# Performance work log

Hardware: AMD Instinct MI355X
Metric: run time of the kernel (lower is better)

Reference implementation:

```python
import jax, jax.numpy as jnp
import numpy as np

D_MODEL = 1024
NUM_HEADS = 16
DEPTH = D_MODEL // NUM_HEADS
LN_EPS = 1e-5


def setup_inputs() -> dict:
    key = jax.random.key(0)
    ks = jax.random.split(key, 12)
    B, S, D = 4, 2048, D_MODEL
    s = 1.0 / np.sqrt(D)
    inp = {
        "Q": jax.random.normal(ks[0], (B, S, D), jnp.float32),
        "K": jax.random.normal(ks[1], (B, S, D), jnp.float32),
        "V": jax.random.normal(ks[2], (B, S, D), jnp.float32),
        "mask": jnp.ones((B, 1, 1, S), jnp.int32),
        "Wq": jax.random.normal(ks[3], (D, D), jnp.float32) * s,
        "bq": jnp.zeros((D,), jnp.float32),
        "Wk": jax.random.normal(ks[4], (D, D), jnp.float32) * s,
        "bk": jnp.zeros((D,), jnp.float32),
        "Wv": jax.random.normal(ks[5], (D, D), jnp.float32) * s,
        "bv": jnp.zeros((D,), jnp.float32),
        "Wo": jax.random.normal(ks[6], (D, D), jnp.float32) * s,
        "bo": jnp.zeros((D,), jnp.float32),
        "gamma": jnp.ones((D,), jnp.float32),
        "beta": jnp.zeros((D,), jnp.float32),
    }
    return inp


def _split_heads(x, B, S):
    # (B, S, D) -> (B, H, S, depth)
    return x.reshape(B, S, NUM_HEADS, DEPTH).transpose(0, 2, 1, 3)


def reference(Q, K, V, mask, Wq, bq, Wk, bk, Wv, bv, Wo, bo, gamma, beta):
    B, S, D = Q.shape
    q = _split_heads(Q @ Wq.T + bq, B, S)  # (B,H,S,dh)
    k = _split_heads(K @ Wk.T + bk, B, S)
    v = _split_heads(V @ Wv.T + bv, B, S)
    scores = jnp.einsum('bhqd,bhkd->bhqk', q, k) / jnp.sqrt(jnp.asarray(DEPTH, q.dtype))
    scores = jnp.where(mask == 0, jnp.asarray(-1e9, scores.dtype), scores)
    attn = jax.nn.softmax(scores, axis=-1)
    ctx = jnp.einsum('bhqk,bhkd->bhqd', attn, v)            # (B,H,S,dh)
    ctx = ctx.transpose(0, 2, 1, 3).reshape(B, S, D)        # merge heads
    out = ctx @ Wo.T + bo
    # residual with the input Q + LayerNorm
    x = out + Q
    mu = jnp.mean(x, axis=-1, keepdims=True)
    var = jnp.mean(jnp.square(x - mu), axis=-1, keepdims=True)
    return gamma * (x - mu) * jax.lax.rsqrt(var + LN_EPS) + beta
```

## Files before the change

kernel.cpp:

```cpp
#include <hip/hip_runtime.h>

#define SEQ 2048
#define BB 4
#define DM 1024
#define NH 16
#define DH 64
#define ROWS (BB*SEQ)

#define BM 128
#define BN 128
#define BK 32
#define KSTEPS (DM / BK)

#define KVBLK 64
#define NT (SEQ / KVBLK)
#define NBUF 3

typedef _Float16 f16;
typedef _Float16 f16x8 __attribute__((ext_vector_type(8)));
typedef _Float16 f16x4 __attribute__((ext_vector_type(4)));
typedef __fp16 h2 __attribute__((ext_vector_type(2)));
typedef float f32x4 __attribute__((ext_vector_type(4)));
typedef float f32x16 __attribute__((ext_vector_type(16)));
typedef unsigned u32x4 __attribute__((ext_vector_type(4)));

__device__ __forceinline__ f32x4 mfma16(f16x8 a, f16x8 b, f32x4 c) {
    return __builtin_amdgcn_mfma_f32_16x16x32_f16(a, b, c, 0, 0, 0);
}
__device__ __forceinline__ f32x16 mfma32(f16x8 a, f16x8 b, f32x16 c) {
    return __builtin_amdgcn_mfma_f32_32x32x16_f16(a, b, c, 0, 0, 0);
}
__device__ __forceinline__ unsigned pkh(float a, float b) {
    auto h = __builtin_amdgcn_cvt_pkrtz(a, b);
    return __builtin_bit_cast(unsigned, h);
}
__device__ __forceinline__ float sum2(unsigned w, float acc) {
    h2 one = { (__fp16)1.0f, (__fp16)1.0f };
    return __builtin_amdgcn_fdot2(__builtin_bit_cast(h2, w), one, acc, false);
}
__device__ __forceinline__ void plswap(unsigned& a, unsigned& b) {
    auto r = __builtin_amdgcn_permlane32_swap((int)a, (int)b, false, false);
    a = (unsigned)r[0];
    b = (unsigned)r[1];
}
__device__ __forceinline__ float2 plswapf(float x) {
    int xi = __builtin_bit_cast(int, x);
    auto r = __builtin_amdgcn_permlane32_swap(xi, xi, false, false);
    return float2{ __builtin_bit_cast(float, (int)r[0]), __builtin_bit_cast(float, (int)r[1]) };
}
typedef const __attribute__((address_space(1))) void gvoid;
typedef __attribute__((address_space(3))) void lvoid;
__device__ __forceinline__ void gload16(const f16* g, f16* l) {
    __builtin_amdgcn_global_load_lds((gvoid*)g, (lvoid*)l, 16, 0, 0);
}

__global__ __launch_bounds__(256) void cvt_weights(
    const float* __restrict__ wq, const float* __restrict__ wk,
    const float* __restrict__ wv, const float* __restrict__ wo,
    f16* __restrict__ oq, f16* __restrict__ ok,
    f16* __restrict__ ov, f16* __restrict__ oo,
    const int* __restrict__ mask, unsigned* __restrict__ pm) {
    if (blockIdx.x == 0) {
        int tid = threadIdx.x;
        const int* mp = mask + (size_t)tid * 32;
        unsigned bits = 0;
#pragma unroll
        for (int j = 0; j < 32; ++j) bits |= (mp[j] != 0 ? 1u : 0u) << j;
        pm[tid] = bits;
    }
    int i = (blockIdx.x * 256 + threadIdx.x) * 4;
    float4 a = *(const float4*)(wq + i);
    float4 b = *(const float4*)(wk + i);
    float4 c = *(const float4*)(wv + i);
    float4 d = *(const float4*)(wo + i);
    f16x4 va = { (f16)a.x, (f16)a.y, (f16)a.z, (f16)a.w };
    f16x4 vb = { (f16)b.x, (f16)b.y, (f16)b.z, (f16)b.w };
    f16x4 vc = { (f16)c.x, (f16)c.y, (f16)c.z, (f16)c.w };
    f16x4 vd = { (f16)d.x, (f16)d.y, (f16)d.z, (f16)d.w };
    *(f16x4*)(oq + i) = va;
    *(f16x4*)(ok + i) = vb;
    *(f16x4*)(ov + i) = vc;
    *(f16x4*)(oo + i) = vd;
}

__global__ __launch_bounds__(256, 3) void gemm_proj3(
    const float* __restrict__ Qf, const float* __restrict__ Kf,
    const float* __restrict__ Vf,
    const f16* __restrict__ wq, const f16* __restrict__ wk,
    const f16* __restrict__ wv,
    const float* __restrict__ bq, const float* __restrict__ bk,
    const float* __restrict__ bv,
    f16* __restrict__ q16o, f16* __restrict__ k16o, f16* __restrict__ v16o,
    float qscale) {
    const float* A; const f16* W; const float* bias; f16* out;
    float scale; int mode;
    if (blockIdx.z == 0)      { A = Qf; W = wq; bias = bq; out = q16o; scale = qscale; mode = 0; }
    else if (blockIdx.z == 1) { A = Kf; W = wk; bias = bk; out = k16o; scale = 1.0f;   mode = 0; }
    else                      { A = Vf; W = wv; bias = bv; out = v16o; scale = 1.0f;   mode = 2; }

    __shared__ f16 lds_a[2][BM][BK + 8];
    __shared__ f16 lds_b[2][BN][BK];
    const int tid = threadIdx.x;
    const int lane = tid & 63;
    const int wv_ = tid >> 6;
    const int wr = wv_ >> 1, wc = wv_ & 1;
    const int lo = lane & 15, hi = lane >> 4;
    const int rowbase = blockIdx.x * BM;
    const int colbase = blockIdx.y * BN;
    const int ar = tid >> 1;
    const int ac = (tid & 1) * 16;

    f32x4 acc[4][4];
#pragma unroll
    for (int m = 0; m < 4; ++m)
#pragma unroll
        for (int n = 0; n < 4; ++n) acc[m][n] = (f32x4){0.f, 0.f, 0.f, 0.f};

    float4 av0, av1, av2, av3;
#define LOAD_A(k0)                                                                  \
    {                                                                               \
        const float* ap_ = A + (size_t)(rowbase + ar) * DM + (k0) + ac;             \
        av0 = *(const float4*)(ap_);                                                \
        av1 = *(const float4*)(ap_ + 4);                                            \
        av2 = *(const float4*)(ap_ + 8);                                            \
        av3 = *(const float4*)(ap_ + 12);                                           \
    }
#define WRITE_A(buf)                                                                \
    {                                                                               \
        f16* dp_ = &lds_a[buf][ar][ac];                                             \
        u32x4 t0_ = { pkh(av0.x, av0.y), pkh(av0.z, av0.w),                         \
                      pkh(av1.x, av1.y), pkh(av1.z, av1.w) };                       \
        u32x4 t1_ = { pkh(av2.x, av2.y), pkh(av2.z, av2.w),                         \
                      pkh(av3.x, av3.y), pkh(av3.z, av3.w) };                       \
        *(u32x4*)(dp_) = t0_;                                                       \
        *(u32x4*)(dp_ + 8) = t1_;                                                   \
    }
#define STAGE_W(buf, k0)                                                            \
    {                                                                               \
        int r_ = lane >> 2;                                                         \
        int kc_ = (((lane & 3) ^ ((r_ >> 1) & 3))) * 8;                             \
        gload16(W + (size_t)(colbase + wv_ * 16 + r_) * DM + (k0) + kc_,            \
                &lds_b[buf][wv_ * 16][0]);                                          \
        gload16(W + (size_t)(colbase + (wv_ + 4) * 16 + r_) * DM + (k0) + kc_,      \
                &lds_b[buf][(wv_ + 4) * 16][0]);                                    \
    }

    LOAD_A(0)
    STAGE_W(0, 0)
    WRITE_A(0)
    __syncthreads();
    int buf = 0;
    for (int ks = 0; ks < KSTEPS; ++ks) {
        if (ks + 1 < KSTEPS) {
            LOAD_A((ks + 1) * BK)
            STAGE_W(buf ^ 1, (ks + 1) * BK)
        }
        f16x8 af[4], bf[4];
#pragma unroll
        for (int m = 0; m < 4; ++m)
            af[m] = *(const f16x8*)&lds_a[buf][wr * 64 + m * 16 + lo][hi * 8];
#pragma unroll
        for (int n = 0; n < 4; ++n) {
            int Rn = wc * 64 + n * 16 + lo;
            bf[n] = *(const f16x8*)&lds_b[buf][Rn][(hi ^ ((Rn >> 1) & 3)) * 8];
        }
#pragma unroll
        for (int m = 0; m < 4; ++m)
#pragma unroll
            for (int n = 0; n < 4; ++n)
                acc[m][n] = mfma16(af[m], bf[n], acc[m][n]);
        if (ks + 1 < KSTEPS) WRITE_A(buf ^ 1)
        __syncthreads();
        buf ^= 1;
    }
#undef LOAD_A
#undef WRITE_A
#undef STAGE_W

    if (mode == 2) {
        f16* tb = &lds_b[0][0][0];
        const int ccolw = wc * 16 + lo;
#pragma unroll
        for (int n = 0; n < 4; ++n) {
            __syncthreads();
            float bv_ = bias[colbase + wc * 64 + n * 16 + lo];
#pragma unroll
            for (int m = 0; m < 4; ++m)
#pragma unroll
                for (int r = 0; r < 4; ++r) {
                    int rowl = wr * 64 + m * 16 + hi * 4 + r;
                    tb[ccolw * 136 + rowl] = (f16)((acc[m][n][r] + bv_) * scale);
                }
            __syncthreads();
            int ccol = tid >> 3;
            int r0 = (tid & 7) * 16;
            int colg = colbase + (ccol >> 4) * 64 + n * 16 + (ccol & 15);
            int hh = colg >> 6, dh = colg & 63;
            int row = rowbase + r0;
            int bi = row >> 11, ss = row & (SEQ - 1);
            f16* dst = out + (((size_t)(bi * NH + hh) * DH + dh) * SEQ + ss);
            f16x8 v0 = *(const f16x8*)&tb[ccol * 136 + r0];
            f16x8 v1 = *(const f16x8*)&tb[ccol * 136 + r0 + 8];
            *(f16x8*)(dst) = v0;
            *(f16x8*)(dst + 8) = v1;
        }
    } else {
#pragma unroll
        for (int n = 0; n < 4; ++n) {
            int col = colbase + wc * 64 + n * 16 + lo;
            float bv_ = bias[col];
            int hh = col >> 6, dh = col & 63;
#pragma unroll
            for (int m = 0; m < 4; ++m)
#pragma unroll
                for (int r = 0; r < 4; ++r) {
                    int row = rowbase + wr * 64 + m * 16 + hi * 4 + r;
                    int bi = row >> 11;
                    int ss = row & (SEQ - 1);
                    float v = (acc[m][n][r] + bv_) * scale;
                    out[(((size_t)(bi * NH + hh) * SEQ + ss) * DH + dh)] = (f16)v;
                }
        }
    }
}

__global__ __launch_bounds__(256, 3) void gemm_oproj(
    const f16* __restrict__ A, const f16* __restrict__ W,
    const float* __restrict__ bo, const float* __restrict__ Qin,
    float* __restrict__ out) {
    __shared__ f16 lds_a[2][BM][BK];
    __shared__ f16 lds_b[2][BN][BK];
    const int lane = threadIdx.x & 63;
    const int wv = threadIdx.x >> 6;
    const int wr = wv >> 1, wc = wv & 1;
    const int lo = lane & 15, hi = lane >> 4;
    const int rowbase = blockIdx.x * BM;
    const int colbase = blockIdx.y * BN;

    f32x4 acc[4][4];
#pragma unroll
    for (int m = 0; m < 4; ++m)
#pragma unroll
        for (int n = 0; n < 4; ++n) acc[m][n] = (f32x4){0.f, 0.f, 0.f, 0.f};

#define STAGE_TILES(buf, k0)                                                        \
    {                                                                               \
        int r_ = lane >> 2;                                                         \
        int kc_ = (((lane & 3) ^ ((r_ >> 1) & 3))) * 8;                             \
        gload16(A + (size_t)(rowbase + wv * 16 + r_) * DM + (k0) + kc_,             \
                &lds_a[buf][wv * 16][0]);                                           \
        gload16(A + (size_t)(rowbase + (wv + 4) * 16 + r_) * DM + (k0) + kc_,       \
                &lds_a[buf][(wv + 4) * 16][0]);                                     \
        gload16(W + (size_t)(colbase + wv * 16 + r_) * DM + (k0) + kc_,             \
                &lds_b[buf][wv * 16][0]);                                           \
        gload16(W + (size_t)(colbase + (wv + 4) * 16 + r_) * DM + (k0) + kc_,       \
                &lds_b[buf][(wv + 4) * 16][0]);                                     \
    }

    STAGE_TILES(0, 0)
    __syncthreads();
    int buf = 0;
    for (int ks = 0; ks < KSTEPS; ++ks) {
        if (ks + 1 < KSTEPS) STAGE_TILES(buf ^ 1, (ks + 1) * BK)
        f16x8 af[4], bf[4];
#pragma unroll
        for (int m = 0; m < 4; ++m) {
            int Rm = wr * 64 + m * 16 + lo;
            af[m] = *(const f16x8*)&lds_a[buf][Rm][(hi ^ ((Rm >> 1) & 3)) * 8];
        }
#pragma unroll
        for (int n = 0; n < 4; ++n) {
            int Rn = wc * 64 + n * 16 + lo;
            bf[n] = *(const f16x8*)&lds_b[buf][Rn][(hi ^ ((Rn >> 1) & 3)) * 8];
        }
#pragma unroll
        for (int m = 0; m < 4; ++m)
#pragma unroll
            for (int n = 0; n < 4; ++n)
                acc[m][n] = mfma16(af[m], bf[n], acc[m][n]);
        __syncthreads();
        buf ^= 1;
    }
#undef STAGE_TILES

#pragma unroll
    for (int n = 0; n < 4; ++n) {
        int col = colbase + wc * 64 + n * 16 + lo;
        float bv = bo[col];
#pragma unroll
        for (int m = 0; m < 4; ++m)
#pragma unroll
            for (int r = 0; r < 4; ++r) {
                int row = rowbase + wr * 64 + m * 16 + hi * 4 + r;
                size_t idx = (size_t)row * DM + col;
                out[idx] = acc[m][n][r] + bv + Qin[idx];
            }
    }
}

__global__ __launch_bounds__(256, 3) void attn_kernel(
    const f16* __restrict__ q16, const f16* __restrict__ k16,
    const f16* __restrict__ v16t, const unsigned* __restrict__ pm,
    f16* __restrict__ out16) {
    __shared__ f16 smem[NBUF][2][KVBLK * 64];
    const int tid = threadIdx.x;
    const int lane = tid & 63;
    const int wv = tid >> 6;
    const int lo = lane & 31, hw = lane >> 5;
    const int bh = blockIdx.y;
    const int b = bh >> 4, hd = bh & 15;
    const int q0 = blockIdx.x * 128 + wv * 32;

    const f16* qp = q16 + ((size_t)bh * SEQ + q0 + lo) * DH + hw * 8;
    const f16* kp = k16 + (size_t)bh * SEQ * DH;
    const f16* vp = v16t + (size_t)bh * DH * SEQ;
    const unsigned* pmb = pm + b * 64;

    const int sr = lane >> 3, scb = lane & 7;
    const int cb = scb ^ sr;

    f16x8 qb[4];
#pragma unroll
    for (int c = 0; c < 4; ++c) qb[c] = *(const f16x8*)(qp + c * 16);

    f32x16 fz;
#pragma unroll
    for (int i = 0; i < 16; ++i) fz[i] = 0.f;
    f32x16 ctx0 = fz, ctx1 = fz;
    float la = 0.f, lb = 0.f;

#define STAGE(buf, KB)                                                              \
    {                                                                               \
        gload16(kp + (size_t)((KB) + wv * 8 + sr) * DH + cb * 8,                    \
                &smem[buf][0][wv * 512]);                                           \
        gload16(kp + (size_t)((KB) + 32 + wv * 8 + sr) * DH + cb * 8,               \
                &smem[buf][0][(4 + wv) * 512]);                                     \
        gload16(vp + (size_t)(wv * 8 + sr) * SEQ + (KB) + cb * 8,                   \
                &smem[buf][1][wv * 512]);                                           \
        gload16(vp + (size_t)(32 + wv * 8 + sr) * SEQ + (KB) + cb * 8,              \
                &smem[buf][1][(4 + wv) * 512]);                                     \
    }

    STAGE(0, 0)
    STAGE(1, KVBLK)

    int bc = 0;
    for (int t = 0; t < NT; ++t) {
        if (t < NT - 1) asm volatile("s_waitcnt vmcnt(4)" ::: "memory");
        else            asm volatile("s_waitcnt vmcnt(0)" ::: "memory");
        __builtin_amdgcn_s_barrier();
        asm volatile("" ::: "memory");

        const f16* kbase = &smem[bc][0][0];
        const f16* vbase = &smem[bc][1][0];

        if (t + 2 < NT) {
            int bs = bc + 2; if (bs >= NBUF) bs -= NBUF;
            STAGE(bs, (t + 2) * KVBLK)
        }

        unsigned bmw0 = pmb[2 * t];
        unsigned bmw1 = pmb[2 * t + 1];

#pragma unroll
        for (int kt = 0; kt < 2; ++kt) {
            f16x8 kf0 = *(const f16x8*)&kbase[(kt * 32 + lo) * 64 + (((0 + hw) ^ (lo & 7)) << 3)];
            f16x8 kf1 = *(const f16x8*)&kbase[(kt * 32 + lo) * 64 + (((2 + hw) ^ (lo & 7)) << 3)];

            f32x16 st;
            __builtin_amdgcn_s_setprio(1);
            st = mfma32(kf0, qb[0], fz);
            f16x8 kf2 = *(const f16x8*)&kbase[(kt * 32 + lo) * 64 + (((4 + hw) ^ (lo & 7)) << 3)];
            st = mfma32(kf1, qb[1], st);
            f16x8 kf3 = *(const f16x8*)&kbase[(kt * 32 + lo) * 64 + (((6 + hw) ^ (lo & 7)) << 3)];
            st = mfma32(kf2, qb[2], st);
            st = mfma32(kf3, qb[3], st);
            __builtin_amdgcn_s_setprio(0);

            unsigned bm = kt ? bmw1 : bmw0;
            if (bm != 0xffffffffu) {
                unsigned bs_ = bm >> (hw * 4);
#pragma unroll
                for (int r = 0; r < 16; ++r)
                    if (!((bs_ >> ((r & 3) + 8 * (r >> 2))) & 1)) st[r] = -1e9f;
            }

#pragma unroll
            for (int i = 0; i < 16; ++i) st[i] = __builtin_amdgcn_exp2f(st[i]);

            __builtin_amdgcn_s_setprio(1);
            {
                unsigned w0 = pkh(st[0], st[1]),   w1 = pkh(st[2], st[3]);
                unsigned w2 = pkh(st[4], st[5]),   w3 = pkh(st[6], st[7]);
                unsigned w4 = pkh(st[8], st[9]),   w5 = pkh(st[10], st[11]);
                unsigned w6 = pkh(st[12], st[13]), w7 = pkh(st[14], st[15]);
                la = sum2(w0, la); lb = sum2(w1, lb);
                la = sum2(w2, la); lb = sum2(w3, lb);
                la = sum2(w4, la); lb = sum2(w5, lb);
                la = sum2(w6, la); lb = sum2(w7, lb);
                f16x8 vf00 = *(const f16x8*)&vbase[(0 * 32 + lo) * 64 + (((kt * 4 + 0 + hw) ^ (lo & 7)) << 3)];
                f16x8 vf10 = *(const f16x8*)&vbase[(1 * 32 + lo) * 64 + (((kt * 4 + 0 + hw) ^ (lo & 7)) << 3)];
                {
                    unsigned a0 = w0, b0 = w2; plswap(a0, b0);
                    unsigned a1 = w1, b1 = w3; plswap(a1, b1);
                    u32x4 t_ = { a0, a1, b0, b1 };
                    f16x8 pb = __builtin_bit_cast(f16x8, t_);
                    ctx0 = mfma32(vf00, pb, ctx0);
                    ctx1 = mfma32(vf10, pb, ctx1);
                }
                f16x8 vf01 = *(const f16x8*)&vbase[(0 * 32 + lo) * 64 + (((kt * 4 + 2 + hw) ^ (lo & 7)) << 3)];
                f16x8 vf11 = *(const f16x8*)&vbase[(1 * 32 + lo) * 64 + (((kt * 4 + 2 + hw) ^ (lo & 7)) << 3)];
                {
                    unsigned a0 = w4, b0 = w6; plswap(a0, b0);
                    unsigned a1 = w5, b1 = w7; plswap(a1, b1);
                    u32x4 t_ = { a0, a1, b0, b1 };
                    f16x8 pb = __builtin_bit_cast(f16x8, t_);
                    ctx0 = mfma32(vf01, pb, ctx0);
                    ctx1 = mfma32(vf11, pb, ctx1);
                }
            }
            __builtin_amdgcn_s_setprio(0);
        }

        bc = (bc + 1 == NBUF) ? 0 : bc + 1;
    }
#undef STAGE

    __syncthreads();

    float lown = la + lb;
    float2 lp = plswapf(lown);
    float rl = 1.0f / (lp.x + lp.y);
    f16* tbp = &smem[0][0][0] + wv * (32 * 66);
#pragma unroll
    for (int u = 0; u < 8; ++u) {
        int d0 = 2 * (u & 1) + 8 * (u >> 1) + 4 * hw;
        unsigned pw0 = pkh(ctx0[2 * u] * rl, ctx0[2 * u + 1] * rl);
        unsigned pw1 = pkh(ctx1[2 * u] * rl, ctx1[2 * u + 1] * rl);
        *(unsigned*)&tbp[lo * 66 + d0] = pw0;
        *(unsigned*)&tbp[lo * 66 + 32 + d0] = pw1;
    }
    __syncthreads();
#pragma unroll
    for (int it = 0; it < 4; ++it) {
        int r = it * 8 + (lane >> 3);
        const unsigned* src = (const unsigned*)(tbp + r * 66);
        int cc = (lane & 7) * 4;
        u32x4 t = { src[cc], src[cc + 1], src[cc + 2], src[cc + 3] };
        f16x8 vvv = __builtin_bit_cast(f16x8, t);
        *(f16x8*)(out16 + ((size_t)(b * SEQ) + q0 + r) * DM + hd * 64 + (lane & 7) * 8) = vvv;
    }
}

__global__ __launch_bounds__(256) void ln_kernel(
    float* __restrict__ x, const float* __restrict__ gamma,
    const float* __restrict__ beta) {
    const int lane = threadIdx.x & 63;
    const int wave = threadIdx.x >> 6;
    const int row = blockIdx.x * 4 + wave;
    float* rp = x + (size_t)row * DM;

    float4 v[4];
#pragma unroll
    for (int j = 0; j < 4; ++j) v[j] = ((const float4*)rp)[lane + 64 * j];

    float sum = 0.f;
#pragma unroll
    for (int j = 0; j < 4; ++j) sum += v[j].x + v[j].y + v[j].z + v[j].w;
#pragma unroll
    for (int off = 1; off < 64; off <<= 1) sum += __shfl_xor(sum, off);
    float mean = sum * (1.f / DM);

    float vs = 0.f;
#pragma unroll
    for (int j = 0; j < 4; ++j) {
        float dx = v[j].x - mean, dy = v[j].y - mean, dz = v[j].z - mean, dw = v[j].w - mean;
        vs += dx * dx + dy * dy + dz * dz + dw * dw;
    }
#pragma unroll
    for (int off = 1; off < 64; off <<= 1) vs += __shfl_xor(vs, off);
    float rstd = rsqrtf(vs * (1.f / DM) + 1e-5f);

#pragma unroll
    for (int j = 0; j < 4; ++j) {
        int idx = lane + 64 * j;
        float4 g = ((const float4*)gamma)[idx];
        float4 bt = ((const float4*)beta)[idx];
        float4 o;
        o.x = (v[j].x - mean) * rstd * g.x + bt.x;
        o.y = (v[j].y - mean) * rstd * g.y + bt.y;
        o.z = (v[j].z - mean) * rstd * g.z + bt.z;
        o.w = (v[j].w - mean) * rstd * g.w + bt.w;
        ((float4*)rp)[idx] = o;
    }
}

extern "C" void kernel_launch(void* const* d_in, const int* in_sizes, int n_in,
                              void* d_out, int out_size, void* d_ws, size_t ws_size,
                              hipStream_t stream) {
    const float* Q    = (const float*)d_in[0];
    const float* K    = (const float*)d_in[1];
    const float* V    = (const float*)d_in[2];
    const int*   mask = (const int*)d_in[3];
    const float* Wq   = (const float*)d_in[4];
    const float* bq   = (const float*)d_in[5];
    const float* Wk   = (const float*)d_in[6];
    const float* bk   = (const float*)d_in[7];
    const float* Wv   = (const float*)d_in[8];
    const float* bv   = (const float*)d_in[9];
    const float* Wo   = (const float*)d_in[10];
    const float* bo   = (const float*)d_in[11];
    const float* gamma = (const float*)d_in[12];
    const float* beta  = (const float*)d_in[13];
    float* out = (float*)d_out;

    char* ws = (char*)d_ws;
    const size_t MB = 1024 * 1024;
    f16* wq16 = (f16*)(ws + 0 * MB);
    f16* wk16 = (f16*)(ws + 2 * MB);
    f16* wv16 = (f16*)(ws + 4 * MB);
    f16* wo16 = (f16*)(ws + 6 * MB);
    f16* c16  = (f16*)(ws + 8 * MB);
    f16* q16  = (f16*)(ws + 24 * MB);
    f16* k16  = (f16*)(ws + 40 * MB);
    f16* v16t = (f16*)(ws + 56 * MB);

    unsigned* pm = (unsigned*)((char*)d_out + (size_t)out_size * 4 - 4096);

    cvt_weights<<<dim3(DM * DM / (256 * 4)), dim3(256), 0, stream>>>(
        Wq, Wk, Wv, Wo, wq16, wk16, wv16, wo16, mask, pm);

    const float qscale = 0.125f * 1.44269504f;

    gemm_proj3<<<dim3(ROWS / BM, DM / BN, 3), dim3(256), 0, stream>>>(
        Q, K, V, wq16, wk16, wv16, bq, bk, bv, q16, k16, v16t, qscale);

    attn_kernel<<<dim3(SEQ / 128, BB * NH), dim3(256), 0, stream>>>(
        q16, k16, v16t, pm, c16);

    gemm_oproj<<<dim3(ROWS / BM, DM / BN), dim3(256), 0, stream>>>(
        c16, wo16, bo, Q, out);

    ln_kernel<<<dim3(ROWS / 4), dim3(256), 0, stream>>>(out, gamma, beta);
}
```

Before: 237.2 us.

## Prefetch A tiles two steps ahead with ping-pong registers and fine-grained waitcnt

The projection GEMM main loop now loads the fp32 A tile two K-steps ahead into alternating register sets. It replaces __syncthreads with an explicit s_waitcnt vmcnt(4) plus s_barrier, so the next A loads stay outstanding while the barrier completes. The aim is to hide global load latency that the previous single-step prefetch exposed. This costs extra registers and relies on the exact count of outstanding vector memory ops, which is fragile if the compiler reorders or splits loads.

```diff
diff --git a/kernel.cpp b/kernel.cpp
--- a/kernel.cpp
+++ b/kernel.cpp
@@ -116,22 +116,23 @@
 #pragma unroll
         for (int n = 0; n < 4; ++n) acc[m][n] = (f32x4){0.f, 0.f, 0.f, 0.f};
 
-    float4 av0, av1, av2, av3;
-#define LOAD_A(k0)                                                                  \
+    float4 avP0, avP1, avP2, avP3;
+    float4 avQ0, avQ1, avQ2, avQ3;
+#define LOAD_A(V0, V1, V2, V3, k0)                                                  \
     {                                                                               \
         const float* ap_ = A + (size_t)(rowbase + ar) * DM + (k0) + ac;             \
-        av0 = *(const float4*)(ap_);                                                \
-        av1 = *(const float4*)(ap_ + 4);                                            \
-        av2 = *(const float4*)(ap_ + 8);                                            \
-        av3 = *(const float4*)(ap_ + 12);                                           \
-    }
-#define WRITE_A(buf)                                                                \
+        V0 = *(const float4*)(ap_);                                                 \
+        V1 = *(const float4*)(ap_ + 4);                                             \
+        V2 = *(const float4*)(ap_ + 8);                                             \
+        V3 = *(const float4*)(ap_ + 12);                                            \
+    }
+#define WRITE_A(buf, V0, V1, V2, V3)                                                \
     {                                                                               \
         f16* dp_ = &lds_a[buf][ar][ac];                                             \
-        u32x4 t0_ = { pkh(av0.x, av0.y), pkh(av0.z, av0.w),                         \
-                      pkh(av1.x, av1.y), pkh(av1.z, av1.w) };                       \
-        u32x4 t1_ = { pkh(av2.x, av2.y), pkh(av2.z, av2.w),                         \
-                      pkh(av3.x, av3.y), pkh(av3.z, av3.w) };                       \
+        u32x4 t0_ = { pkh(V0.x, V0.y), pkh(V0.z, V0.w),                             \
+                      pkh(V1.x, V1.y), pkh(V1.z, V1.w) };                           \
+        u32x4 t1_ = { pkh(V2.x, V2.y), pkh(V2.z, V2.w),                             \
+                      pkh(V3.x, V3.y), pkh(V3.z, V3.w) };                           \
         *(u32x4*)(dp_) = t0_;                                                       \
         *(u32x4*)(dp_ + 8) = t1_;                                                   \
     }
@@ -145,37 +146,53 @@
                 &lds_b[buf][(wv_ + 4) * 16][0]);                                    \
     }
 
-    LOAD_A(0)
+    LOAD_A(avP0, avP1, avP2, avP3, 0)
+    WRITE_A(0, avP0, avP1, avP2, avP3)
     STAGE_W(0, 0)
-    WRITE_A(0)
-    __syncthreads();
+    LOAD_A(avP0, avP1, avP2, avP3, BK)
+    asm volatile("s_waitcnt vmcnt(4) lgkmcnt(0)" ::: "memory");
+    __builtin_amdgcn_s_barrier();
+    asm volatile("" ::: "memory");
+
     int buf = 0;
-    for (int ks = 0; ks < KSTEPS; ++ks) {
-        if (ks + 1 < KSTEPS) {
-            LOAD_A((ks + 1) * BK)
-            STAGE_W(buf ^ 1, (ks + 1) * BK)
-        }
-        f16x8 af[4], bf[4];
-#pragma unroll
-        for (int m = 0; m < 4; ++m)
-            af[m] = *(const f16x8*)&lds_a[buf][wr * 64 + m * 16 + lo][hi * 8];
-#pragma unroll
-        for (int n = 0; n < 4; ++n) {
-            int Rn = wc * 64 + n * 16 + lo;
-            bf[n] = *(const f16x8*)&lds_b[buf][Rn][(hi ^ ((Rn >> 1) & 3)) * 8];
-        }
-#pragma unroll
-        for (int m = 0; m < 4; ++m)
-#pragma unroll
-            for (int n = 0; n < 4; ++n)
-                acc[m][n] = mfma16(af[m], bf[n], acc[m][n]);
-        if (ks + 1 < KSTEPS) WRITE_A(buf ^ 1)
-        __syncthreads();
-        buf ^= 1;
+#define GITER(ks, AC0, AC1, AC2, AC3, AN0, AN1, AN2, AN3)                           \
+    {                                                                               \
+        if ((ks) + 1 < KSTEPS) STAGE_W(buf ^ 1, ((ks) + 1) * BK)                    \
+        if ((ks) + 2 < KSTEPS) LOAD_A(AN0, AN1, AN2, AN3, ((ks) + 2) * BK)          \
+        f16x8 af[4], bf[4];                                                         \
+        _Pragma("unroll")                                                           \
+        for (int m = 0; m < 4; ++m)                                                 \
+            af[m] = *(const f16x8*)&lds_a[buf][wr * 64 + m * 16 + lo][hi * 8];      \
+        _Pragma("unroll")                                                           \
+        for (int n = 0; n < 4; ++n) {                                               \
+            int Rn = wc * 64 + n * 16 + lo;                                         \
+            bf[n] = *(const f16x8*)&lds_b[buf][Rn][(hi ^ ((Rn >> 1) & 3)) * 8];     \
+        }                                                                           \
+        _Pragma("unroll")                                                           \
+        for (int m = 0; m < 4; ++m)                                                 \
+            _Pragma("unroll")                                                       \
+            for (int n = 0; n < 4; ++n)                                             \
+                acc[m][n] = mfma16(af[m], bf[n], acc[m][n]);                        \
+        if ((ks) + 1 < KSTEPS) {                                                    \
+            WRITE_A(buf ^ 1, AC0, AC1, AC2, AC3)                                    \
+            if ((ks) + 2 < KSTEPS)                                                  \
+                asm volatile("s_waitcnt vmcnt(4) lgkmcnt(0)" ::: "memory");         \
+            else                                                                    \
+                asm volatile("s_waitcnt vmcnt(0) lgkmcnt(0)" ::: "memory");         \
+            __builtin_amdgcn_s_barrier();                                           \
+            asm volatile("" ::: "memory");                                          \
+        }                                                                           \
+        buf ^= 1;                                                                   \
+    }
+
+    for (int ks = 0; ks < KSTEPS; ks += 2) {
+        GITER(ks,     avP0, avP1, avP2, avP3, avQ0, avQ1, avQ2, avQ3)
+        GITER(ks + 1, avQ0, avQ1, avQ2, avQ3, avP0, avP1, avP2, avP3)
     }
 #undef LOAD_A
 #undef WRITE_A
 #undef STAGE_W
+#undef GITER
 
     if (mode == 2) {
         f16* tb = &lds_b[0][0][0];
```

After: 232.0 us. -2.2%, faster.
